# Kernel tuning notes

Hardware: AMD Instinct MI355X
Metric: run time of the kernel (lower is better)

The kernel has to match this reference:

```python
import jax, jax.numpy as jnp
import numpy as np

EMBED_DIM = 1024
HEAD_DIM = 128
SEQ = 2048
BATCH = 16


def setup_inputs() -> dict:
    key = jax.random.key(0)
    ks = jax.random.split(key, 7)
    s = 1.0 / np.sqrt(EMBED_DIM)
    return {
        "x": jax.random.normal(ks[0], (BATCH, SEQ, EMBED_DIM), dtype=jnp.float32),
        "Wq": jax.random.uniform(ks[1], (EMBED_DIM, HEAD_DIM), jnp.float32, -s, s),
        "bq": jax.random.uniform(ks[2], (HEAD_DIM,), jnp.float32, -s, s),
        "Wk": jax.random.uniform(ks[3], (EMBED_DIM, HEAD_DIM), jnp.float32, -s, s),
        "bk": jax.random.uniform(ks[4], (HEAD_DIM,), jnp.float32, -s, s),
        "Wv": jax.random.uniform(ks[5], (EMBED_DIM, HEAD_DIM), jnp.float32, -s, s),
        "bv": jax.random.uniform(ks[6], (HEAD_DIM,), jnp.float32, -s, s),
    }


def reference(x, Wq, bq, Wk, bk, Wv, bv):
    # q,k,v: [B,S,Dh]
    q = x @ Wq + bq
    k = x @ Wk + bk
    v = x @ Wv + bv
    # NOTE: original module MULTIPLIES by embed_dim**0.5 (faithful to source).
    scale = jnp.asarray(EMBED_DIM ** 0.5, dtype=x.dtype)
    scores = jnp.einsum("bqd,bkd->bqk", q, k) * scale  # [B,S,S]
    causal = jnp.tril(jnp.ones((SEQ, SEQ), dtype=bool))
    scores = jnp.where(causal, scores, -jnp.inf)
    attn = jax.nn.softmax(scores, axis=-1)
    # dropout_rate=0 -> identity
    return jnp.einsum("bqk,bkd->bqd", attn, v)
```

## Files before the change

kernel.cpp:

```cpp
#include <hip/hip_runtime.h>

#define BATCH 16
#define SEQ   2048
#define EMB   1024
#define DH    128

typedef _Float16 half4_t __attribute__((ext_vector_type(4)));
typedef _Float16 half8_t __attribute__((ext_vector_type(8)));
typedef float    f32x4   __attribute__((ext_vector_type(4)));

#define OFF_WT2 0u
#define OFF_QHI 0x200000u
#define OFF_QLO (OFF_QHI + 0x800000u)
#define OFF_KHI (OFF_QLO + 0x800000u)
#define OFF_KLO (OFF_KHI + 0x800000u)
#define OFF_VT  (OFF_KLO + 0x800000u)

__device__ __forceinline__ void gload16(const void* g, void* l) {
    __builtin_amdgcn_global_load_lds(
        (__attribute__((address_space(1))) const unsigned int*)g,
        (__attribute__((address_space(3))) unsigned int*)l, 16, 0, 0);
}

__global__ __launch_bounds__(256) void prep_w(
    const float* __restrict__ Wq, const float* __restrict__ Wk,
    const float* __restrict__ Wv, _Float16* __restrict__ Wt2) {
    const int t  = blockIdx.x * 256 + threadIdx.x;
    const int kc = t / 2560, rem = t % 2560;
    const int lo = rem >= 1536 ? 1 : 0;
    const int rr = lo ? rem - 1536 : rem;
    const int nt = rr >> 6, c = rr & 63;
    const int g = c >> 4, r = c & 15;
    const int k0 = kc * 32 + g * 8;
    const float* W; int col;
    if (nt < 8)       { W = Wq; col = nt * 16 + r; }
    else if (nt < 16) { W = Wk; col = (nt - 8) * 16 + r; }
    else              { W = Wv; col = (nt - 16) * 16 + r; }
    half8_t v;
#pragma unroll
    for (int j = 0; j < 8; ++j) {
        float f = W[(size_t)(k0 + j) * DH + col];
        _Float16 h = (_Float16)f;
        v[j] = lo ? (_Float16)(f - (float)h) : h;
    }
    *(half8_t*)((char*)Wt2 + (size_t)kc * 40960 + (lo ? 24576 : 0)
                + (size_t)nt * 1024 + c * 16) = v;
}

#define XBUF  0
#define FHI   65536
#define FLO   81920

__global__ __launch_bounds__(512, 2) void proj_qkv(
    const float* __restrict__ x, const _Float16* __restrict__ Wt2,
    const float* __restrict__ bq, const float* __restrict__ bk,
    const float* __restrict__ bv,
    char* __restrict__ qhi, char* __restrict__ qlo,
    char* __restrict__ khi, char* __restrict__ klo,
    char* __restrict__ vt) {
    __shared__ __align__(16) char lds[98304];
    const int tid = threadIdx.x, lane = tid & 63, w = tid >> 6;
    const int l15 = lane & 15, g = lane >> 4;
    const int m0  = blockIdx.x * 128;

    f32x4 acc[8][3];
#pragma unroll
    for (int mt = 0; mt < 8; ++mt)
#pragma unroll
        for (int j = 0; j < 3; ++j) acc[mt][j] = {};

    auto stage_x = [&](int t, int buf) {
#pragma unroll
        for (int i = 0; i < 4; ++i) {
            const int cb = w * 256 + i * 64;
            const int sidx = cb + lane;
            const int r = sidx >> 4, s = sidx & 15;
            const int c = s ^ (r & 7);
            gload16(x + (size_t)(m0 + r) * EMB + t * 64 + c * 4,
                    lds + XBUF + buf * 32768 + cb * 16);
        }
    };

    auto loadW = [&](int kc, half8_t& qh, half8_t& ql, half8_t& kh,
                     half8_t& kl, half8_t& vh) {
        const char* p = (const char*)Wt2 + (size_t)kc * 40960 + lane * 16;
        qh = *(const half8_t*)(p + (size_t)w * 1024);
        ql = *(const half8_t*)(p + 24576 + (size_t)w * 1024);
        kh = *(const half8_t*)(p + (size_t)(8 + w) * 1024);
        kl = *(const half8_t*)(p + 24576 + (size_t)(8 + w) * 1024);
        vh = *(const half8_t*)(p + (size_t)(16 + w) * 1024);
    };

    auto compute = [&](int s, const half8_t& qh, const half8_t& ql,
                       const half8_t& kh, const half8_t& kl, const half8_t& vh) {
#pragma unroll
        for (int mt = 0; mt < 8; ++mt) {
            const int RR = mt * 16 + l15;
            const int sl = ((s * 4 + g) ^ (l15 & 7)) * 16;
            half8_t xh = *(const half8_t*)(lds + FHI + RR * 128 + sl);
            half8_t xl = *(const half8_t*)(lds + FLO + RR * 128 + sl);
            acc[mt][0] = __builtin_amdgcn_mfma_f32_16x16x32_f16(xh, qh, acc[mt][0], 0, 0, 0);
            acc[mt][0] = __builtin_amdgcn_mfma_f32_16x16x32_f16(xl, qh, acc[mt][0], 0, 0, 0);
            acc[mt][0] = __builtin_amdgcn_mfma_f32_16x16x32_f16(xh, ql, acc[mt][0], 0, 0, 0);
            acc[mt][1] = __builtin_amdgcn_mfma_f32_16x16x32_f16(xh, kh, acc[mt][1], 0, 0, 0);
            acc[mt][1] = __builtin_amdgcn_mfma_f32_16x16x32_f16(xl, kh, acc[mt][1], 0, 0, 0);
            acc[mt][1] = __builtin_amdgcn_mfma_f32_16x16x32_f16(xh, kl, acc[mt][1], 0, 0, 0);
            acc[mt][2] = __builtin_amdgcn_mfma_f32_16x16x32_f16(xh, vh, acc[mt][2], 0, 0, 0);
        }
    };

    stage_x(0, 0);

    for (int t = 0; t < 16; ++t) {
        __syncthreads();

        half8_t qh0, ql0, kh0, kl0, vh0, qh1, ql1, kh1, kl1, vh1;
        loadW(2 * t,     qh0, ql0, kh0, kl0, vh0);
        loadW(2 * t + 1, qh1, ql1, kh1, kl1, vh1);
        __builtin_amdgcn_sched_barrier(0);

#pragma unroll
        for (int u = 0; u < 2; ++u) {
            const char* Xb = lds + XBUF + (t & 1) * 32768;
            const int task = tid + u * 512;
            const int R = task >> 3;
            const int o = task & 7;
            const int rx = R & 7;
            f32x4 a0 = *(const f32x4*)(Xb + R * 256 + ((o * 2)     ^ rx) * 16);
            f32x4 a1 = *(const f32x4*)(Xb + R * 256 + ((o * 2 + 1) ^ rx) * 16);
            half8_t hi, lo;
#pragma unroll
            for (int jj = 0; jj < 4; ++jj) {
                float f = a0[jj]; _Float16 h = (_Float16)f;
                hi[jj] = h; lo[jj] = (_Float16)(f - (float)h);
                float f2 = a1[jj]; _Float16 h2 = (_Float16)f2;
                hi[jj + 4] = h2; lo[jj + 4] = (_Float16)(f2 - (float)h2);
            }
            *(half8_t*)(lds + FHI + R * 128 + (o ^ rx) * 16) = hi;
            *(half8_t*)(lds + FLO + R * 128 + (o ^ rx) * 16) = lo;
        }

        asm volatile("" :: "v"(qh0), "v"(ql0), "v"(kh0), "v"(kl0), "v"(vh0));
        asm volatile("" :: "v"(qh1), "v"(ql1), "v"(kh1), "v"(kl1), "v"(vh1));

        __syncthreads();

        if (t < 15) stage_x(t + 1, (t + 1) & 1);
        __builtin_amdgcn_sched_barrier(0);

        compute(0, qh0, ql0, kh0, kl0, vh0);
        compute(1, qh1, ql1, kh1, kl1, vh1);
    }

    __syncthreads();
    float* scr = (float*)(lds + (size_t)w * 1280);
    const float SC = 46.166241308446828f;

#pragma unroll
    for (int j = 0; j < 3; ++j) {
        float bias;
        if (j == 0)      bias = bq[w * 16 + l15];
        else if (j == 1) bias = bk[w * 16 + l15];
        else             bias = bv[w * 16 + l15];
#pragma unroll
        for (int mt = 0; mt < 8; ++mt) {
            f32x4 a = acc[mt][j];
#pragma unroll
            for (int r = 0; r < 4; ++r) {
                float v = a[r] + bias;
                if (j == 0) v *= SC;
                scr[(g * 4 + r) * 20 + l15] = v;
            }
            if (j < 2) {
                f32x4 tv = *(const f32x4*)(scr + l15 * 20 + g * 4);
                half4_t h4, l4;
#pragma unroll
                for (int r = 0; r < 4; ++r) {
                    _Float16 h = (_Float16)tv[r];
                    h4[r] = h; l4[r] = (_Float16)(tv[r] - (float)h);
                }
                const int tIdx = blockIdx.x * 8 + mt;
                const int octm = 2 * w + (g >> 1);
                const size_t off = (size_t)tIdx * 4096 + (octm >> 2) * 1024
                                 + (octm & 3) * 256 + l15 * 16 + (g & 1) * 8;
                char* dh_ = (j == 0) ? qhi : khi;
                char* dl_ = (j == 0) ? qlo : klo;
                *(half4_t*)(dh_ + off) = h4;
                *(half4_t*)(dl_ + off) = l4;
            } else {
                half4_t v4;
#pragma unroll
                for (int r = 0; r < 4; ++r)
                    v4[r] = (_Float16)scr[(g * 4 + r) * 20 + l15];
                const int s0 = (m0 & (SEQ - 1)) + mt * 16;
                const int b  = m0 >> 11;
                const size_t off = ((size_t)b * 64 + (s0 >> 5)) * 8192
                                 + ((s0 >> 4) & 1) * 4096 + (size_t)w * 512
                                 + g * 128 + l15 * 8;
                *(half4_t*)(vt + off) = v4;
            }
        }
    }
}

__global__ __launch_bounds__(512) void attn(
    const char* __restrict__ qhi, const char* __restrict__ qlo,
    const char* __restrict__ khi, const char* __restrict__ klo,
    const char* __restrict__ vt, float* __restrict__ out) {
    __shared__ __align__(16) char lds[49152];
    const int tid = threadIdx.x, lane = tid & 63, w = tid >> 6;
    const int l15 = lane & 15, g = lane >> 4;
    const int gid = blockIdx.x;
    const int b   = ((gid & 7) << 1) | ((gid >> 3) & 1);
    const int pr  = gid >> 4;
    const int jt  = (w < 4) ? (31 - pr) : pr;
    const int wq  = w & 3;
    const int qw0 = jt * 64 + wq * 16;
    const int nkv = 2 * (32 - pr);

    auto stage = [&](int t, int buf) {
        char* dst = lds + buf * 24576;
        const size_t kb4 = ((size_t)b * 128 + t * 2) * 4096;
        const size_t vb8 = ((size_t)b * 64 + t) * 8192;
        const int off = w * 1024;
        gload16(khi + kb4 + off + lane * 16, dst + off);
        gload16(klo + kb4 + off + lane * 16, dst + 8192 + off);
        gload16(vt  + vb8 + off + lane * 16, dst + 16384 + off);
    };

    const size_t qt4 = ((size_t)b * 128 + (qw0 >> 4)) * 4096;
    half8_t Qh[4], Ql[4];
#pragma unroll
    for (int kk = 0; kk < 4; ++kk) {
        const size_t o = qt4 + kk * 1024 + g * 256 + l15 * 16;
        Qh[kk] = *(const half8_t*)(qhi + o);
        Ql[kk] = *(const half8_t*)(qlo + o);
    }

    f32x4 o[8];
#pragma unroll
    for (int dt = 0; dt < 8; ++dt) o[dt] = {};
    float mrun = -3.0e38f, ell = 0.0f;

    stage(0, 0);

    for (int t = 0; t < nkv; ++t) {
        __syncthreads();
        if (t + 1 < nkv) stage(t + 1, (t + 1) & 1);

        const int kb = t * 32;
        if (kb <= qw0 + 15) {
            const char* kbuf = lds + (t & 1) * 24576;

            f32x4 sa0 = {}, sb0 = {}, sa1 = {}, sb1 = {};
            __builtin_amdgcn_s_setprio(1);
#pragma unroll
            for (int kk = 0; kk < 4; ++kk) {
                const int fo = kk * 1024 + g * 256 + l15 * 16;
                half8_t kh0 = *(const half8_t*)(kbuf + fo);
                half8_t kl0 = *(const half8_t*)(kbuf + 8192 + fo);
                half8_t kh1 = *(const half8_t*)(kbuf + 4096 + fo);
                half8_t kl1 = *(const half8_t*)(kbuf + 12288 + fo);
                sa0 = __builtin_amdgcn_mfma_f32_16x16x32_f16(kh0, Qh[kk], sa0, 0, 0, 0);
                sb0 = __builtin_amdgcn_mfma_f32_16x16x32_f16(kl0, Qh[kk], sb0, 0, 0, 0);
                sb0 = __builtin_amdgcn_mfma_f32_16x16x32_f16(kh0, Ql[kk], sb0, 0, 0, 0);
                sa1 = __builtin_amdgcn_mfma_f32_16x16x32_f16(kh1, Qh[kk], sa1, 0, 0, 0);
                sb1 = __builtin_amdgcn_mfma_f32_16x16x32_f16(kl1, Qh[kk], sb1, 0, 0, 0);
                sb1 = __builtin_amdgcn_mfma_f32_16x16x32_f16(kh1, Ql[kk], sb1, 0, 0, 0);
            }
            __builtin_amdgcn_s_setprio(0);
            f32x4 s0 = sa0 + sb0, s1 = sa1 + sb1;

            if (kb + 31 > qw0) {
#pragma unroll
                for (int r = 0; r < 4; ++r) {
                    if (kb + g * 4 + r      > qw0 + l15) s0[r] = -3.0e38f;
                    if (kb + 16 + g * 4 + r > qw0 + l15) s1[r] = -3.0e38f;
                }
            }

            float mt = fmaxf(fmaxf(fmaxf(s0[0], s0[1]), fmaxf(s0[2], s0[3])),
                             fmaxf(fmaxf(s1[0], s1[1]), fmaxf(s1[2], s1[3])));
            mt = fmaxf(mt, __shfl_xor(mt, 16, 64));
            mt = fmaxf(mt, __shfl_xor(mt, 32, 64));
            if (!__all(mt <= mrun + 8.0f)) {
                const float mnew = fmaxf(mrun, mt);
                const float alpha = exp2f(mrun - mnew);
                ell *= alpha;
#pragma unroll
                for (int dt = 0; dt < 8; ++dt) o[dt] *= alpha;
                mrun = mnew;
            }
            float p[8];
#pragma unroll
            for (int r = 0; r < 4; ++r) {
                p[r]     = exp2f(s0[r] - mrun);
                p[4 + r] = exp2f(s1[r] - mrun);
            }
            float ps = ((p[0] + p[1]) + (p[2] + p[3])) + ((p[4] + p[5]) + (p[6] + p[7]));
            ps += __shfl_xor(ps, 16, 64);
            ps += __shfl_xor(ps, 32, 64);
            ell += ps;

            half4_t pf0, pf1;
#pragma unroll
            for (int r = 0; r < 4; ++r) { pf0[r] = (_Float16)p[r]; pf1[r] = (_Float16)p[4 + r]; }

            const char* vbuf = kbuf + 16384;
            __builtin_amdgcn_s_setprio(1);
#pragma unroll
            for (int dt = 0; dt < 8; ++dt) {
                const int vo = dt * 512 + g * 128 + l15 * 8;
                half4_t v0 = *(const half4_t*)(vbuf + vo);
                half4_t v1 = *(const half4_t*)(vbuf + 4096 + vo);
                o[dt] = __builtin_amdgcn_mfma_f32_16x16x16f16(v0, pf0, o[dt], 0, 0, 0);
                o[dt] = __builtin_amdgcn_mfma_f32_16x16x16f16(v1, pf1, o[dt], 0, 0, 0);
            }
            __builtin_amdgcn_s_setprio(0);
        }
    }

    const float rinv = 1.0f / ell;
    float* orow = out + ((size_t)b * SEQ + qw0 + l15) * DH + g * 4;
#pragma unroll
    for (int dt = 0; dt < 8; ++dt) {
        f32x4 ov = o[dt] * rinv;
        *(f32x4*)(orow + dt * 16) = ov;
    }
}

extern "C" void kernel_launch(void* const* d_in, const int* in_sizes, int n_in,
                              void* d_out, int out_size, void* d_ws, size_t ws_size,
                              hipStream_t stream) {
    const float* x  = (const float*)d_in[0];
    const float* Wq = (const float*)d_in[1];
    const float* bq = (const float*)d_in[2];
    const float* Wk = (const float*)d_in[3];
    const float* bk = (const float*)d_in[4];
    const float* Wv = (const float*)d_in[5];
    const float* bv = (const float*)d_in[6];
    float* out = (float*)d_out;

    char* ws = (char*)d_ws;
    _Float16* Wt2 = (_Float16*)(ws + OFF_WT2);
    char* q_hi = ws + OFF_QHI;
    char* q_lo = ws + OFF_QLO;
    char* k_hi = ws + OFF_KHI;
    char* k_lo = ws + OFF_KLO;
    char* v_t  = ws + OFF_VT;

    prep_w  <<<320, 256, 0, stream>>>(Wq, Wk, Wv, Wt2);
    proj_qkv<<<256, 512, 0, stream>>>(x, Wt2, bq, bk, bv, q_hi, q_lo, k_hi, k_lo, v_t);
    attn    <<<256, 512, 0, stream>>>(q_hi, q_lo, k_hi, k_lo, v_t, out);
}
```

Before: 140.9 us.

## Stage projection weights through LDS with async loads and halve K-step

The QKV projection kernel now stages the split-fp16 weight tile into a double-buffered LDS region with global_load_lds, alongside x, instead of loading weights directly into registers at the top of each iteration. The K step shrinks from 64 to 32, giving twice as many iterations with smaller x and fp16 staging buffers. This aims to hide weight-load latency behind compute, but it raises LDS use to 128 KB per block, which may drop occupancy below the two blocks per CU requested, and it doubles the barriers.

New measurement: 140.0 us. About the same (-0.6%).

```diff
diff --git a/kernel.cpp b/kernel.cpp
--- a/kernel.cpp
+++ b/kernel.cpp
@@ -48,8 +48,9 @@
 }
 
 #define XBUF  0
-#define FHI   65536
-#define FLO   81920
+#define WBUF  32768
+#define FHI   114688
+#define FLO   122880
 
 __global__ __launch_bounds__(512, 2) void proj_qkv(
     const float* __restrict__ x, const _Float16* __restrict__ Wt2,
@@ -58,7 +59,7 @@
     char* __restrict__ qhi, char* __restrict__ qlo,
     char* __restrict__ khi, char* __restrict__ klo,
     char* __restrict__ vt) {
-    __shared__ __align__(16) char lds[98304];
+    __shared__ __align__(16) char lds[131072];
     const int tid = threadIdx.x, lane = tid & 63, w = tid >> 6;
     const int l15 = lane & 15, g = lane >> 4;
     const int m0  = blockIdx.x * 128;
@@ -71,34 +72,38 @@
 
     auto stage_x = [&](int t, int buf) {
 #pragma unroll
-        for (int i = 0; i < 4; ++i) {
-            const int cb = w * 256 + i * 64;
+        for (int i = 0; i < 2; ++i) {
+            const int cb = w * 128 + i * 64;
             const int sidx = cb + lane;
-            const int r = sidx >> 4, s = sidx & 15;
+            const int r = sidx >> 3, s = sidx & 7;
             const int c = s ^ (r & 7);
-            gload16(x + (size_t)(m0 + r) * EMB + t * 64 + c * 4,
-                    lds + XBUF + buf * 32768 + cb * 16);
+            gload16(x + (size_t)(m0 + r) * EMB + t * 32 + c * 4,
+                    lds + XBUF + buf * 16384 + cb * 16);
         }
     };
 
-    auto loadW = [&](int kc, half8_t& qh, half8_t& ql, half8_t& kh,
-                     half8_t& kl, half8_t& vh) {
-        const char* p = (const char*)Wt2 + (size_t)kc * 40960 + lane * 16;
-        qh = *(const half8_t*)(p + (size_t)w * 1024);
-        ql = *(const half8_t*)(p + 24576 + (size_t)w * 1024);
-        kh = *(const half8_t*)(p + (size_t)(8 + w) * 1024);
-        kl = *(const half8_t*)(p + 24576 + (size_t)(8 + w) * 1024);
-        vh = *(const half8_t*)(p + (size_t)(16 + w) * 1024);
+    auto stage_w = [&](int t, int buf) {
+        const char* wsrc = (const char*)Wt2 + (size_t)t * 40960;
+#pragma unroll
+        for (int i = 0; i < 5; ++i) {
+            const int off = (w * 5 + i) * 1024;
+            gload16(wsrc + off + lane * 16, lds + WBUF + buf * 40960 + off);
+        }
     };
 
-    auto compute = [&](int s, const half8_t& qh, const half8_t& ql,
-                       const half8_t& kh, const half8_t& kl, const half8_t& vh) {
+    auto compute = [&](int buf) {
+        const char* wb = lds + WBUF + buf * 40960;
+        half8_t qh = *(const half8_t*)(wb + (size_t)w * 1024 + lane * 16);
+        half8_t ql = *(const half8_t*)(wb + 24576 + (size_t)w * 1024 + lane * 16);
+        half8_t kh = *(const half8_t*)(wb + (size_t)(8 + w) * 1024 + lane * 16);
+        half8_t kl = *(const half8_t*)(wb + 24576 + (size_t)(8 + w) * 1024 + lane * 16);
+        half8_t vh = *(const half8_t*)(wb + (size_t)(16 + w) * 1024 + lane * 16);
 #pragma unroll
         for (int mt = 0; mt < 8; ++mt) {
             const int RR = mt * 16 + l15;
-            const int sl = ((s * 4 + g) ^ (l15 & 7)) * 16;
-            half8_t xh = *(const half8_t*)(lds + FHI + RR * 128 + sl);
-            half8_t xl = *(const half8_t*)(lds + FLO + RR * 128 + sl);
+            const int sl = (g ^ ((RR >> 1) & 3)) * 16;
+            half8_t xh = *(const half8_t*)(lds + FHI + RR * 64 + sl);
+            half8_t xl = *(const half8_t*)(lds + FLO + RR * 64 + sl);
             acc[mt][0] = __builtin_amdgcn_mfma_f32_16x16x32_f16(xh, qh, acc[mt][0], 0, 0, 0);
             acc[mt][0] = __builtin_amdgcn_mfma_f32_16x16x32_f16(xl, qh, acc[mt][0], 0, 0, 0);
             acc[mt][0] = __builtin_amdgcn_mfma_f32_16x16x32_f16(xh, ql, acc[mt][0], 0, 0, 0);
@@ -110,24 +115,18 @@
     };
 
     stage_x(0, 0);
-
-    for (int t = 0; t < 16; ++t) {
+    stage_w(0, 0);
+
+    for (int t = 0; t < 32; ++t) {
         __syncthreads();
 
-        half8_t qh0, ql0, kh0, kl0, vh0, qh1, ql1, kh1, kl1, vh1;
-        loadW(2 * t,     qh0, ql0, kh0, kl0, vh0);
-        loadW(2 * t + 1, qh1, ql1, kh1, kl1, vh1);
-        __builtin_amdgcn_sched_barrier(0);
-
-#pragma unroll
-        for (int u = 0; u < 2; ++u) {
-            const char* Xb = lds + XBUF + (t & 1) * 32768;
-            const int task = tid + u * 512;
-            const int R = task >> 3;
-            const int o = task & 7;
+        {
+            const char* Xb = lds + XBUF + (t & 1) * 16384;
+            const int R = tid >> 2;
+            const int s = tid & 3;
             const int rx = R & 7;
-            f32x4 a0 = *(const f32x4*)(Xb + R * 256 + ((o * 2)     ^ rx) * 16);
-            f32x4 a1 = *(const f32x4*)(Xb + R * 256 + ((o * 2 + 1) ^ rx) * 16);
+            f32x4 a0 = *(const f32x4*)(Xb + R * 128 + ((2 * s)     ^ rx) * 16);
+            f32x4 a1 = *(const f32x4*)(Xb + R * 128 + ((2 * s + 1) ^ rx) * 16);
             half8_t hi, lo;
 #pragma unroll
             for (int jj = 0; jj < 4; ++jj) {
@@ -136,20 +135,19 @@
                 float f2 = a1[jj]; _Float16 h2 = (_Float16)f2;
                 hi[jj + 4] = h2; lo[jj + 4] = (_Float16)(f2 - (float)h2);
             }
-            *(half8_t*)(lds + FHI + R * 128 + (o ^ rx) * 16) = hi;
-            *(half8_t*)(lds + FLO + R * 128 + (o ^ rx) * 16) = lo;
-        }
-
-        asm volatile("" :: "v"(qh0), "v"(ql0), "v"(kh0), "v"(kl0), "v"(vh0));
-        asm volatile("" :: "v"(qh1), "v"(ql1), "v"(kh1), "v"(kl1), "v"(vh1));
-
+            const int sw = (s ^ ((R >> 1) & 3)) * 16;
+            *(half8_t*)(lds + FHI + R * 64 + sw) = hi;
+            *(half8_t*)(lds + FLO + R * 64 + sw) = lo;
+        }
         __syncthreads();
 
-        if (t < 15) stage_x(t + 1, (t + 1) & 1);
+        if (t < 31) {
+            stage_x(t + 1, (t + 1) & 1);
+            stage_w(t + 1, (t + 1) & 1);
+        }
         __builtin_amdgcn_sched_barrier(0);
 
-        compute(0, qh0, ql0, kh0, kl0, vh0);
-        compute(1, qh1, ql1, kh1, kl1, vh1);
+        compute(t & 1);
     }
 
     __syncthreads();
```
